# Kernel optimization log

Hardware: AMD Instinct MI355X
Metric: run time of the kernel (lower is better)

## Reference

```python
import jax, jax.numpy as jnp
import numpy as np

B = 2048


def _maxpool2(x):
    return jax.lax.reduce_window(x, -jnp.inf, jax.lax.max,
                                 (1, 1, 2, 2), (1, 1, 2, 2), 'VALID')


def setup_inputs() -> dict:
    key = jax.random.key(0)
    ks = jax.random.split(key, 7)
    return {
        'x': jax.random.normal(ks[0], (B, 3, 32, 32), dtype=jnp.float32),
        'conv_w': jax.random.normal(ks[1], (45, 1, 5, 5), dtype=jnp.float32),
        'conv_b': jax.random.normal(ks[2], (45,), dtype=jnp.float32) * 0.1,
        'tree_w': jax.random.normal(ks[3], (1, 16, 15, 3, 7, 7, 2, 2), dtype=jnp.float32),
        'tree_b': jax.random.normal(ks[4], (1, 16, 3, 7), dtype=jnp.float32),
        'fc_w': jax.random.normal(ks[5], (10, 336), dtype=jnp.float32),
        'fc_b': jax.random.normal(ks[6], (10,), dtype=jnp.float32) * 0.1,
    }


def reference(x, conv_w, conv_b, tree_w, tree_b, fc_w, fc_b):
    # grouped conv: in=3, groups=3, out=45, kernel 5x5, VALID -> (B,45,28,28)
    out = jax.lax.conv_general_dilated(
        x, conv_w, window_strides=(1, 1), padding='VALID',
        dimension_numbers=('NCHW', 'OIHW', 'NCHW'), feature_group_count=3)
    out = jax.nn.sigmoid(out + conv_b[None, :, None, None])
    out = _maxpool2(out)  # (B,45,14,14)
    b = out.shape[0]
    # unfold((2,2),stride=2) + the torch reshape/transpose chain is equivalent to:
    # (B,45,14,14) -> (b, g=3, m=15, i=7, ki=2, j=7, kj=2) -> (b,m,g,i,j,ki,kj)
    xt = out.reshape(b, 3, 15, 7, 2, 7, 2).transpose(0, 2, 1, 3, 5, 4, 6)
    # TreeLayer: elementwise mul with weights (16,m,g,i,j,ki,kj) then sum over m,j,ki,kj
    t = jnp.einsum('bmgijkl,fmgijkl->bfgi', xt, tree_w[0]) + tree_b  # (B,16,3,7)
    t = jax.nn.sigmoid(t)
    return t.reshape(b, 16 * 3 * 7) @ fc_w.T + fc_b  # (B,10)
```

## Files before the change

kernel.cpp:

```cpp
#include <hip/hip_runtime.h>
#include <hip/hip_fp16.h>

#define BATCH 2048

typedef _Float16 f16x8 __attribute__((ext_vector_type(8)));
typedef float f32x4 __attribute__((ext_vector_type(4)));

__device__ __forceinline__ float sigmoidf(float v) {
    return 1.0f / (1.0f + __expf(-v));
}

#define WS_W3B  0
#define WS_FCW  301056

__global__ __launch_bounds__(256) void k_prep(
    const float* __restrict__ tree_w,
    const float* __restrict__ fc_w,
    ushort* __restrict__ W3B,
    float* __restrict__ FCW2)
{
    int pidx = blockIdx.x * 256 + threadIdx.x;
    if (pidx < 18816) {
        int gi = pidx / 896;
        int rem = pidx - gi * 896;
        int c = rem >> 6, lane2 = rem & 63;
        int f = lane2 & 15, qq = lane2 >> 4;
        int g = gi / 7, i = gi - g * 7;
        ushort h[8];
        #pragma unroll
        for (int u = 0; u < 8; u++) {
            int k = c * 32 + qq * 8 + u;
            int tt = k >> 6;
            int q2 = (k >> 4) & 3;
            int nn = k & 15;
            int u27 = tt * 4 + q2;
            int ki = u27 / 14;
            int pw = u27 - ki * 14;
            int j = pw >> 1, kj = pw & 1;
            float v = 0.f;
            if (nn < 15)
                v = tree_w[(size_t)f * 8820 + nn * 588 + g * 196 + i * 28
                           + j * 4 + ki * 2 + kj];
            h[u] = __half_as_ushort(__float2half(v));
        }
        *(uint4*)(W3B + (size_t)pidx * 8) = *(uint4*)h;
    } else if (pidx < 22176) {
        int j = pidx - 18816;
        int f = j & 15;
        int r = j >> 4;
        int i = r % 7;
        int r2 = r / 7;
        int o = r2 % 10;
        int g = r2 / 10;
        FCW2[j] = fc_w[o * 336 + f * 21 + g * 7 + i];
    }
}

__global__ __launch_bounds__(256, 4) void kF_all(
    const float* __restrict__ x,
    const float* __restrict__ conv_w,
    const float* __restrict__ conv_b,
    const ushort* __restrict__ W3B,
    const float* __restrict__ FCW2,
    const float* __restrict__ tree_b,
    const float* __restrict__ fc_b,
    float* __restrict__ out)
{
    __shared__ __align__(16) ushort xsc[2 * 4656];
    __shared__ __align__(16) ushort ps[2 * 3192];
    __shared__ __align__(16) ushort tsl[14 * 16];

    const int tid  = threadIdx.x;
    const int blk  = blockIdx.x;
    const int pair = blk / 3;
    const int g    = blk - pair * 3;
    const int img0 = pair * 2;
    const int lane = tid & 63;
    const int n    = lane & 15;
    const int q    = lane >> 4;
    const int wave = tid >> 6;

    #pragma unroll
    for (int im2 = 0; im2 < 2; im2++) {
        float4 v = ((const float4*)(x + (size_t)(img0 + im2) * 3072 + g * 1024))[tid];
        int row = tid >> 3, col = (tid & 7) * 4;
        __half2 a = __float22half2_rn(make_float2(v.x, v.y));
        __half2 b = __float22half2_rn(make_float2(v.z, v.w));
        uint2 pk;
        pk.x = *(unsigned int*)&a;
        pk.y = *(unsigned int*)&b;
        *(uint2*)(xsc + im2 * 4656 + row * 36 + col) = pk;
    }
    if (tid < 64) {
        int im2 = tid >> 5, r = tid & 31;
        *(uint2*)(xsc + im2 * 4656 + r * 36 + 32) = make_uint2(0u, 0u);
    }

    f16x8 B1 = {0, 0, 0, 0, 0, 0, 0, 0};
    f16x8 B2 = {0, 0, 0, 0, 0, 0, 0, 0};
    float bias = 0.f;
    if (n < 15) {
        const float* wrow = conv_w + (g * 15 + n) * 25;
        #pragma unroll
        for (int u = 0; u < 5; u++) B1[u] = (_Float16)wrow[q * 5 + u];
        if (q == 0) {
            #pragma unroll
            for (int u = 0; u < 5; u++) B2[u] = (_Float16)wrow[20 + u];
        }
        bias = conv_b[g * 15 + n];
    }
    __syncthreads();

    for (int t = tid; t < 1728; t += 256) {
        int im2 = t / 864;
        int rem = t - im2 * 864;
        int s = rem / 288 + 1;
        int rem2 = rem - (s - 1) * 288;
        int row = rem2 / 9, g4 = rem2 - row * 9;
        ushort* base = xsc + im2 * 4656;
        ushort* dst = base + s * 1164 + row * 36 + g4 * 4;
        if (g4 == 8) { *(uint2*)dst = make_uint2(0u, 0u); continue; }
        uint2 lo = *(const uint2*)(base + row * 36 + g4 * 4);
        uint2 hi = *(const uint2*)(base + row * 36 + g4 * 4 + 4);
        unsigned int w0 = lo.x, w1 = lo.y, w2 = hi.x, w3 = hi.y;
        unsigned int o0, o1;
        if (s == 1)      { o0 = (w0 >> 16) | (w1 << 16); o1 = (w1 >> 16) | (w2 << 16); }
        else if (s == 2) { o0 = w1;                      o1 = w2; }
        else             { o0 = (w1 >> 16) | (w2 << 16); o1 = (w2 >> 16) | (w3 << 16); }
        *(uint2*)dst = make_uint2(o0, o1);
    }

    const int dr = (n >> 1) & 1, dc = n & 1, n4 = n >> 2;
    const int a2c = 144 - q * 36;
    int aoff[13], svr[13];
    #pragma unroll
    for (int it = 0; it < 13; it++) {
        int t = wave + it * 4;
        int pb = t * 4 + n4;
        int ph = pb / 14, pw = pb - ph * 14;
        int r = 2 * ph + dr, c = 2 * pw + dc;
        int s = c & 3;
        aoff[it] = s * 1164 + (r + q) * 36 + (c - s);
        int i = t / 7, tt = t - i * 7;
        svr[it] = i * 456 + tt * 64 + lane;
    }
    __syncthreads();

    #pragma unroll
    for (int im2 = 0; im2 < 2; im2++) {
        const ushort* xb = xsc + im2 * 4656;
        ushort* pso = ps + im2 * 3192;
        #pragma unroll
        for (int it = 0; it < 12; it++) {
            const ushort* pA = xb + aoff[it];
            union { struct { uint2 a, b; } u; f16x8 v; } A1, A2;
            A1.u.a = *(const uint2*)pA;
            A1.u.b = *(const uint2*)(pA + 4);
            A2.u.a = *(const uint2*)(pA + a2c);
            A2.u.b = *(const uint2*)(pA + a2c + 4);
            f32x4 d = {0.f, 0.f, 0.f, 0.f};
            d = __builtin_amdgcn_mfma_f32_16x16x32_f16(A1.v, B1, d, 0, 0, 0);
            d = __builtin_amdgcn_mfma_f32_16x16x32_f16(A2.v, B2, d, 0, 0, 0);
            float mx = fmaxf(fmaxf(d[0], d[1]), fmaxf(d[2], d[3]));
            float val = (n < 15) ? sigmoidf(mx + bias) : 0.f;
            pso[svr[it]] = __half_as_ushort(__float2half(val));
        }
        if (wave == 0) {
            const ushort* pA = xb + aoff[12];
            union { struct { uint2 a, b; } u; f16x8 v; } A1, A2;
            A1.u.a = *(const uint2*)pA;
            A1.u.b = *(const uint2*)(pA + 4);
            A2.u.a = *(const uint2*)(pA + a2c);
            A2.u.b = *(const uint2*)(pA + a2c + 4);
            f32x4 d = {0.f, 0.f, 0.f, 0.f};
            d = __builtin_amdgcn_mfma_f32_16x16x32_f16(A1.v, B1, d, 0, 0, 0);
            d = __builtin_amdgcn_mfma_f32_16x16x32_f16(A2.v, B2, d, 0, 0, 0);
            float mx = fmaxf(fmaxf(d[0], d[1]), fmaxf(d[2], d[3]));
            float val = (n < 15) ? sigmoidf(mx + bias) : 0.f;
            pso[svr[12]] = __half_as_ushort(__float2half(val));
        }
    }
    __syncthreads();

    for (int ii = wave; ii < 7; ii += 4) {
        const f16x8* Wb = (const f16x8*)W3B + (size_t)(g * 7 + ii) * 896;
        const ushort* ap = ps + (lane & 1) * 3192 + ii * 456;
        f16x8 Bf[14];
        #pragma unroll
        for (int c = 0; c < 14; c++) Bf[c] = Wb[c * 64 + lane];
        f32x4 D0 = {0.f, 0.f, 0.f, 0.f};
        f32x4 D1 = {0.f, 0.f, 0.f, 0.f};
        #pragma unroll
        for (int c = 0; c < 7; c++) {
            f16x8 Ae = *(const f16x8*)(ap + (2 * c) * 32 + q * 8);
            D0 = __builtin_amdgcn_mfma_f32_16x16x32_f16(Ae, Bf[2 * c], D0, 0, 0, 0);
            f16x8 Ao = *(const f16x8*)(ap + (2 * c + 1) * 32 + q * 8);
            D1 = __builtin_amdgcn_mfma_f32_16x16x32_f16(Ao, Bf[2 * c + 1], D1, 0, 0, 0);
        }
        if (q == 0) {
            float tb = tree_b[n * 21 + g * 7 + ii];
            float t0 = (D0[0] + D1[0]) + tb;
            float t1 = (D0[1] + D1[1]) + tb;
            tsl[(0 * 7 + ii) * 16 + n] = __half_as_ushort(__float2half(sigmoidf(t0)));
            tsl[(1 * 7 + ii) * 16 + n] = __half_as_ushort(__float2half(sigmoidf(t1)));
        }
    }
    __syncthreads();

    if (wave == 0 && lane < 20) {
        int im2 = lane / 10, o = lane - (lane / 10) * 10;
        const __half2* tp = (const __half2*)(tsl + im2 * 7 * 16);
        const float4* wp = (const float4*)(FCW2 + (size_t)(g * 10 + o) * 112);
        float acc = (g == 0) ? fc_b[o] : 0.f;
        #pragma unroll
        for (int jj = 0; jj < 28; jj++) {
            float4 w4 = wp[jj];
            float2 p0 = __half22float2(tp[2 * jj]);
            float2 p1 = __half22float2(tp[2 * jj + 1]);
            acc = fmaf(p0.x, w4.x, acc);
            acc = fmaf(p0.y, w4.y, acc);
            acc = fmaf(p1.x, w4.z, acc);
            acc = fmaf(p1.y, w4.w, acc);
        }
#if defined(__HIP_PLATFORM_AMD__)
        unsafeAtomicAdd(out + (size_t)(img0 + im2) * 10 + o, acc);
#else
        atomicAdd(out + (size_t)(img0 + im2) * 10 + o, acc);
#endif
    }
}

extern "C" void kernel_launch(void* const* d_in, const int* in_sizes, int n_in,
                              void* d_out, int out_size, void* d_ws, size_t ws_size,
                              hipStream_t stream) {
    const float* x      = (const float*)d_in[0];
    const float* conv_w = (const float*)d_in[1];
    const float* conv_b = (const float*)d_in[2];
    const float* tree_w = (const float*)d_in[3];
    const float* tree_b = (const float*)d_in[4];
    const float* fc_w   = (const float*)d_in[5];
    const float* fc_b   = (const float*)d_in[6];
    float* out = (float*)d_out;

    ushort* W3B  = (ushort*)((char*)d_ws + WS_W3B);
    float*  FCW2 = (float*)((char*)d_ws + WS_FCW);

    hipMemsetAsync(out, 0, (size_t)BATCH * 10 * sizeof(float), stream);
    k_prep<<<87, 256, 0, stream>>>(tree_w, fc_w, W3B, FCW2);
    kF_all<<<1024 * 3, 256, 0, stream>>>(x, conv_w, conv_b, W3B, FCW2,
                                         tree_b, fc_b, out);
}
```

Baseline: 115.8 us.

## Process four images per block, fuse output zeroing into prep, faster sigmoid

Each block now handles four images per channel group in two rounds of two, so tree-layer weight fragments are loaded once for four images and all four MFMA accumulator rows are used. The output zeroing memset is folded into the prep kernel, saving a launch. Sigmoid uses raw exp2/rcp intrinsics with the bias prescaled, and the shift pass is restructured to compute all three shifts per thread. Shared memory grows and occupancy hint drops to 3, and conv stages are serialized across the two rounds.

```diff
diff --git a/kernel.cpp b/kernel.cpp
--- a/kernel.cpp
+++ b/kernel.cpp
@@ -6,8 +6,8 @@
 typedef _Float16 f16x8 __attribute__((ext_vector_type(8)));
 typedef float f32x4 __attribute__((ext_vector_type(4)));
 
-__device__ __forceinline__ float sigmoidf(float v) {
-    return 1.0f / (1.0f + __expf(-v));
+__device__ __forceinline__ float fast_sigmoid(float v) {
+    return __builtin_amdgcn_rcpf(1.0f + __builtin_amdgcn_exp2f(v * -1.44269504f));
 }
 
 #define WS_W3B  0
@@ -17,9 +17,11 @@
     const float* __restrict__ tree_w,
     const float* __restrict__ fc_w,
     ushort* __restrict__ W3B,
-    float* __restrict__ FCW2)
+    float* __restrict__ FCW2,
+    float* __restrict__ out)
 {
     int pidx = blockIdx.x * 256 + threadIdx.x;
+    if (pidx < 20480) out[pidx] = 0.f;
     if (pidx < 18816) {
         int gi = pidx / 896;
         int rem = pidx - gi * 896;
@@ -56,7 +58,7 @@
     }
 }
 
-__global__ __launch_bounds__(256, 4) void kF_all(
+__global__ __launch_bounds__(256, 3) void kF_all(
     const float* __restrict__ x,
     const float* __restrict__ conv_w,
     const float* __restrict__ conv_b,
@@ -67,38 +69,27 @@
     float* __restrict__ out)
 {
     __shared__ __align__(16) ushort xsc[2 * 4656];
-    __shared__ __align__(16) ushort ps[2 * 3192];
-    __shared__ __align__(16) ushort tsl[14 * 16];
+    __shared__ __align__(16) ushort ps[4 * 3192];
+    __shared__ __align__(16) ushort tsl[28 * 16];
 
     const int tid  = threadIdx.x;
     const int blk  = blockIdx.x;
-    const int pair = blk / 3;
-    const int g    = blk - pair * 3;
-    const int img0 = pair * 2;
+    const int quad = blk / 3;
+    const int g    = blk - quad * 3;
+    const int img0 = quad * 4;
     const int lane = tid & 63;
     const int n    = lane & 15;
     const int q    = lane >> 4;
     const int wave = tid >> 6;
 
+    float4 xv[4];
     #pragma unroll
-    for (int im2 = 0; im2 < 2; im2++) {
-        float4 v = ((const float4*)(x + (size_t)(img0 + im2) * 3072 + g * 1024))[tid];
-        int row = tid >> 3, col = (tid & 7) * 4;
-        __half2 a = __float22half2_rn(make_float2(v.x, v.y));
-        __half2 b = __float22half2_rn(make_float2(v.z, v.w));
-        uint2 pk;
-        pk.x = *(unsigned int*)&a;
-        pk.y = *(unsigned int*)&b;
-        *(uint2*)(xsc + im2 * 4656 + row * 36 + col) = pk;
-    }
-    if (tid < 64) {
-        int im2 = tid >> 5, r = tid & 31;
-        *(uint2*)(xsc + im2 * 4656 + r * 36 + 32) = make_uint2(0u, 0u);
-    }
+    for (int im = 0; im < 4; im++)
+        xv[im] = ((const float4*)(x + (size_t)(img0 + im) * 3072 + g * 1024))[tid];
 
     f16x8 B1 = {0, 0, 0, 0, 0, 0, 0, 0};
     f16x8 B2 = {0, 0, 0, 0, 0, 0, 0, 0};
-    float bias = 0.f;
+    float bs = 0.f;
     if (n < 15) {
         const float* wrow = conv_w + (g * 15 + n) * 25;
         #pragma unroll
@@ -107,27 +98,7 @@
             #pragma unroll
             for (int u = 0; u < 5; u++) B2[u] = (_Float16)wrow[20 + u];
         }
-        bias = conv_b[g * 15 + n];
-    }
-    __syncthreads();
-
-    for (int t = tid; t < 1728; t += 256) {
-        int im2 = t / 864;
-        int rem = t - im2 * 864;
-        int s = rem / 288 + 1;
-        int rem2 = rem - (s - 1) * 288;
-        int row = rem2 / 9, g4 = rem2 - row * 9;
-        ushort* base = xsc + im2 * 4656;
-        ushort* dst = base + s * 1164 + row * 36 + g4 * 4;
-        if (g4 == 8) { *(uint2*)dst = make_uint2(0u, 0u); continue; }
-        uint2 lo = *(const uint2*)(base + row * 36 + g4 * 4);
-        uint2 hi = *(const uint2*)(base + row * 36 + g4 * 4 + 4);
-        unsigned int w0 = lo.x, w1 = lo.y, w2 = hi.x, w3 = hi.y;
-        unsigned int o0, o1;
-        if (s == 1)      { o0 = (w0 >> 16) | (w1 << 16); o1 = (w1 >> 16) | (w2 << 16); }
-        else if (s == 2) { o0 = w1;                      o1 = w2; }
-        else             { o0 = (w1 >> 16) | (w2 << 16); o1 = (w2 >> 16) | (w3 << 16); }
-        *(uint2*)dst = make_uint2(o0, o1);
+        bs = conv_b[g * 15 + n] * -1.44269504f;
     }
 
     const int dr = (n >> 1) & 1, dc = n & 1, n4 = n >> 2;
@@ -144,47 +115,87 @@
         int i = t / 7, tt = t - i * 7;
         svr[it] = i * 456 + tt * 64 + lane;
     }
-    __syncthreads();
+
+    const int rowA = tid / 9, g4A = tid - rowA * 9;
+    const int vB   = tid + 256;
+    const int rowB = vB / 9,  g4B = vB - rowB * 9;
+
+    auto do_shift = [&](int row, int g4) {
+        #pragma unroll
+        for (int im2 = 0; im2 < 2; im2++) {
+            ushort* sp = xsc + im2 * 4656 + row * 36 + g4 * 4;
+            if (g4 == 8) {
+                uint2 z = make_uint2(0u, 0u);
+                *(uint2*)(sp + 1164) = z;
+                *(uint2*)(sp + 2328) = z;
+                *(uint2*)(sp + 3492) = z;
+            } else {
+                uint2 lo = *(const uint2*)sp;
+                uint2 hi = *(const uint2*)(sp + 4);
+                unsigned w0 = lo.x, w1 = lo.y, w2 = hi.x, w3 = hi.y;
+                unsigned t01 = (w0 >> 16) | (w1 << 16);
+                unsigned t12 = (w1 >> 16) | (w2 << 16);
+                unsigned t23 = (w2 >> 16) | (w3 << 16);
+                *(uint2*)(sp + 1164) = make_uint2(t01, t12);
+                *(uint2*)(sp + 2328) = make_uint2(w1, w2);
+                *(uint2*)(sp + 3492) = make_uint2(t12, t23);
+            }
+        }
+    };
+
+    auto conv_tile = [&](int it, const ushort* xb, ushort* pso) {
+        const ushort* pA = xb + aoff[it];
+        union { struct { uint2 a, b; } u; f16x8 v; } A1, A2;
+        A1.u.a = *(const uint2*)pA;
+        A1.u.b = *(const uint2*)(pA + 4);
+        A2.u.a = *(const uint2*)(pA + a2c);
+        A2.u.b = *(const uint2*)(pA + a2c + 4);
+        f32x4 d = {0.f, 0.f, 0.f, 0.f};
+        d = __builtin_amdgcn_mfma_f32_16x16x32_f16(A1.v, B1, d, 0, 0, 0);
+        d = __builtin_amdgcn_mfma_f32_16x16x32_f16(A2.v, B2, d, 0, 0, 0);
+        float mx = fmaxf(fmaxf(d[0], d[1]), fmaxf(d[2], d[3]));
+        float e = __builtin_amdgcn_exp2f(fmaf(mx, -1.44269504f, bs));
+        float val = __builtin_amdgcn_rcpf(1.0f + e);
+        pso[svr[it]] = __half_as_ushort(__float2half(val));
+    };
 
     #pragma unroll
-    for (int im2 = 0; im2 < 2; im2++) {
-        const ushort* xb = xsc + im2 * 4656;
-        ushort* pso = ps + im2 * 3192;
-        #pragma unroll
-        for (int it = 0; it < 12; it++) {
-            const ushort* pA = xb + aoff[it];
-            union { struct { uint2 a, b; } u; f16x8 v; } A1, A2;
-            A1.u.a = *(const uint2*)pA;
-            A1.u.b = *(const uint2*)(pA + 4);
-            A2.u.a = *(const uint2*)(pA + a2c);
-            A2.u.b = *(const uint2*)(pA + a2c + 4);
-            f32x4 d = {0.f, 0.f, 0.f, 0.f};
-            d = __builtin_amdgcn_mfma_f32_16x16x32_f16(A1.v, B1, d, 0, 0, 0);
-            d = __builtin_amdgcn_mfma_f32_16x16x32_f16(A2.v, B2, d, 0, 0, 0);
-            float mx = fmaxf(fmaxf(d[0], d[1]), fmaxf(d[2], d[3]));
-            float val = (n < 15) ? sigmoidf(mx + bias) : 0.f;
-            pso[svr[it]] = __half_as_ushort(__float2half(val));
-        }
-        if (wave == 0) {
-            const ushort* pA = xb + aoff[12];
-            union { struct { uint2 a, b; } u; f16x8 v; } A1, A2;
-            A1.u.a = *(const uint2*)pA;
-            A1.u.b = *(const uint2*)(pA + 4);
-            A2.u.a = *(const uint2*)(pA + a2c);
-            A2.u.b = *(const uint2*)(pA + a2c + 4);
-            f32x4 d = {0.f, 0.f, 0.f, 0.f};
-            d = __builtin_amdgcn_mfma_f32_16x16x32_f16(A1.v, B1, d, 0, 0, 0);
-            d = __builtin_amdgcn_mfma_f32_16x16x32_f16(A2.v, B2, d, 0, 0, 0);
-            float mx = fmaxf(fmaxf(d[0], d[1]), fmaxf(d[2], d[3]));
-            float val = (n < 15) ? sigmoidf(mx + bias) : 0.f;
-            pso[svr[12]] = __half_as_ushort(__float2half(val));
-        }
-    }
-    __syncthreads();
+    for (int r2 = 0; r2 < 2; r2++) {
+        #pragma unroll
+        for (int im2 = 0; im2 < 2; im2++) {
+            float4 v = xv[r2 * 2 + im2];
+            int row = tid >> 3, col = (tid & 7) * 4;
+            __half2 a = __float22half2_rn(make_float2(v.x, v.y));
+            __half2 b = __float22half2_rn(make_float2(v.z, v.w));
+            uint2 pk;
+            pk.x = *(unsigned int*)&a;
+            pk.y = *(unsigned int*)&b;
+            *(uint2*)(xsc + im2 * 4656 + row * 36 + col) = pk;
+        }
+        if (tid < 64) {
+            int im2 = tid >> 5, r = tid & 31;
+            *(uint2*)(xsc + im2 * 4656 + r * 36 + 32) = make_uint2(0u, 0u);
+        }
+        __syncthreads();
+
+        do_shift(rowA, g4A);
+        if (tid < 32) do_shift(rowB, g4B);
+        __syncthreads();
+
+        #pragma unroll
+        for (int im2 = 0; im2 < 2; im2++) {
+            const ushort* xb = xsc + im2 * 4656;
+            ushort* pso = ps + (r2 * 2 + im2) * 3192;
+            #pragma unroll
+            for (int it = 0; it < 12; it++) conv_tile(it, xb, pso);
+            if (wave == 0) conv_tile(12, xb, pso);
+        }
+        __syncthreads();
+    }
 
     for (int ii = wave; ii < 7; ii += 4) {
         const f16x8* Wb = (const f16x8*)W3B + (size_t)(g * 7 + ii) * 896;
-        const ushort* ap = ps + (lane & 1) * 3192 + ii * 456;
+        const ushort* ap = ps + (n & 3) * 3192 + ii * 456;
         f16x8 Bf[14];
         #pragma unroll
         for (int c = 0; c < 14; c++) Bf[c] = Wb[c * 64 + lane];
@@ -199,33 +210,36 @@
         }
         if (q == 0) {
             float tb = tree_b[n * 21 + g * 7 + ii];
-            float t0 = (D0[0] + D1[0]) + tb;
-            float t1 = (D0[1] + D1[1]) + tb;
-            tsl[(0 * 7 + ii) * 16 + n] = __half_as_ushort(__float2half(sigmoidf(t0)));
-            tsl[(1 * 7 + ii) * 16 + n] = __half_as_ushort(__float2half(sigmoidf(t1)));
+            #pragma unroll
+            for (int im = 0; im < 4; im++) {
+                float t = (D0[im] + D1[im]) + tb;
+                tsl[(im * 7 + ii) * 16 + n] =
+                    __half_as_ushort(__float2half(fast_sigmoid(t)));
+            }
         }
     }
     __syncthreads();
 
-    if (wave == 0 && lane < 20) {
-        int im2 = lane / 10, o = lane - (lane / 10) * 10;
-        const __half2* tp = (const __half2*)(tsl + im2 * 7 * 16);
+    if (lane < 10) {
+        const int im4 = wave, o = lane;
+        const uint2* tp = (const uint2*)(tsl + im4 * 112);
         const float4* wp = (const float4*)(FCW2 + (size_t)(g * 10 + o) * 112);
         float acc = (g == 0) ? fc_b[o] : 0.f;
         #pragma unroll
         for (int jj = 0; jj < 28; jj++) {
             float4 w4 = wp[jj];
-            float2 p0 = __half22float2(tp[2 * jj]);
-            float2 p1 = __half22float2(tp[2 * jj + 1]);
+            uint2 hv = tp[jj];
+            float2 p0 = __half22float2(*(const __half2*)&hv.x);
+            float2 p1 = __half22float2(*(const __half2*)&hv.y);
             acc = fmaf(p0.x, w4.x, acc);
             acc = fmaf(p0.y, w4.y, acc);
             acc = fmaf(p1.x, w4.z, acc);
             acc = fmaf(p1.y, w4.w, acc);
         }
 #if defined(__HIP_PLATFORM_AMD__)
-        unsafeAtomicAdd(out + (size_t)(img0 + im2) * 10 + o, acc);
+        unsafeAtomicAdd(out + (size_t)(img0 + im4) * 10 + o, acc);
 #else
-        atomicAdd(out + (size_t)(img0 + im2) * 10 + o, acc);
+        atomicAdd(out + (size_t)(img0 + im4) * 10 + o, acc);
 #endif
     }
 }
@@ -245,8 +259,7 @@
     ushort* W3B  = (ushort*)((char*)d_ws + WS_W3B);
     float*  FCW2 = (float*)((char*)d_ws + WS_FCW);
 
-    hipMemsetAsync(out, 0, (size_t)BATCH * 10 * sizeof(float), stream);
-    k_prep<<<87, 256, 0, stream>>>(tree_w, fc_w, W3B, FCW2);
-    kF_all<<<1024 * 3, 256, 0, stream>>>(x, conv_w, conv_b, W3B, FCW2,
-                                         tree_b, fc_b, out);
-}
+    k_prep<<<87, 256, 0, stream>>>(tree_w, fc_w, W3B, FCW2, out);
+    kF_all<<<512 * 3, 256, 0, stream>>>(x, conv_w, conv_b, W3B, FCW2,
+                                        tree_b, fc_b, out);
+}
```

After: 111.7 us. 3.6% less time.
